# Kernel optimization log

Hardware: AMD Instinct MI355X
Metric: run time of the kernel (lower is better)

Reference implementation:

```python
import jax, jax.numpy as jnp
import numpy as np

B, L, D, H = 4, 2048, 512, 8
HD = D // H
NEG = -1e9


def setup_inputs() -> dict:
    key = jax.random.key(0)
    ks = jax.random.split(key, 11)
    s = 1.0 / np.sqrt(D)
    inp = {
        "q": jax.random.normal(ks[0], (B, L, D), jnp.float32),
        "k": jax.random.normal(ks[1], (B, L, D), jnp.float32),
        "v": jax.random.normal(ks[2], (B, L, D), jnp.float32),
        "mask": jnp.broadcast_to(jnp.tril(jnp.ones((L, L), jnp.int32)), (B, L, L)),
        "Wq": jax.random.normal(ks[3], (D, D), jnp.float32) * s,
        "bq": jax.random.normal(ks[4], (D,), jnp.float32) * s,
        "Wk": jax.random.normal(ks[5], (D, D), jnp.float32) * s,
        "bk": jax.random.normal(ks[6], (D,), jnp.float32) * s,
        "Wv": jax.random.normal(ks[7], (D, D), jnp.float32) * s,
        "bv": jax.random.normal(ks[8], (D,), jnp.float32) * s,
        "Wo": jax.random.normal(ks[9], (D, D), jnp.float32) * s,
        "bo": jax.random.normal(ks[10], (D,), jnp.float32) * s,
    }
    return inp


def reference(q, k, v, mask, Wq, bq, Wk, bk, Wv, bv, Wo, bo):
    # Linear projections (torch Linear: x @ W.T + b)
    Q = (q @ Wq.T + bq).reshape(B, L, H, HD).transpose(0, 2, 1, 3)  # [B,H,L,hd]
    K = (k @ Wk.T + bk).reshape(B, L, H, HD).transpose(0, 2, 1, 3)
    V = (v @ Wv.T + bv).reshape(B, L, H, HD).transpose(0, 2, 1, 3)
    # scaled dot-product attention with masked_fill(mask==0, -1e9)
    score = jnp.einsum('bhqd,bhkd->bhqk', Q, K) / jnp.sqrt(jnp.float32(HD))
    score = jnp.where(mask[:, None, :, :] == 0, NEG, score)
    attn = jax.nn.softmax(score, axis=-1)
    ctx = jnp.einsum('bhqk,bhkd->bhqd', attn, V)  # [B,H,L,hd]
    ctx = ctx.transpose(0, 2, 1, 3).reshape(B, L, D)
    return ctx @ Wo.T + bo
```

## Files before the change

kernel.cpp:

```cpp
#include <hip/hip_runtime.h>
#include <hip/hip_bf16.h>
#include <math.h>

constexpr int Bc  = 4;
constexpr int Lc  = 2048;
constexpr int Dc  = 512;
constexpr int Hc  = 8;
constexpr int HDc = 64;

constexpr int GK = Dc;
constexpr int BK = 64;

typedef __attribute__((ext_vector_type(8))) short bf16x8;
typedef __attribute__((ext_vector_type(4))) short bf16x4;
typedef __attribute__((ext_vector_type(4))) float f32x4;
typedef __attribute__((ext_vector_type(16))) float f32x16;
typedef __attribute__((ext_vector_type(4))) int i32x4;

static __device__ __forceinline__ short f2bf(float x) {
    __hip_bfloat16 h = __float2bfloat16(x);
    return (short)__builtin_bit_cast(unsigned short, h);
}

static __device__ __forceinline__ int cvtpk_bf16(float lo, float hi) {
    int r;
    asm("v_cvt_pk_bf16_f32 %0, %1, %2" : "=v"(r) : "v"(lo), "v"(hi));
    return r;
}

static __device__ __forceinline__ void gload_lds16(const void* g, void* l) {
    __builtin_amdgcn_global_load_lds(
        (const __attribute__((address_space(1))) void*)g,
        (__attribute__((address_space(3))) void*)l, 16, 0, 0);
}

__global__ __launch_bounds__(256)
void cast_all(const float* __restrict__ q, const float* __restrict__ k,
              const float* __restrict__ v, const float* __restrict__ wq,
              const float* __restrict__ wk, const float* __restrict__ wv,
              const float* __restrict__ wo, short* __restrict__ dst) {
    const size_t i = ((size_t)blockIdx.x * 256 + threadIdx.x) * 8;
    const float* src; size_t off;
    if      (i <  4194304) { src = q;  off = i; }
    else if (i <  8388608) { src = k;  off = i -  4194304; }
    else if (i < 12582912) { src = v;  off = i -  8388608; }
    else if (i < 12845056) { src = wq; off = i - 12582912; }
    else if (i < 13107200) { src = wk; off = i - 12845056; }
    else if (i < 13369344) { src = wv; off = i - 13107200; }
    else                   { src = wo; off = i - 13369344; }
    const float4 a = *(const float4*)(src + off);
    const float4 b = *(const float4*)(src + off + 4);
    bf16x8 o;
    o[0] = f2bf(a.x); o[1] = f2bf(a.y); o[2] = f2bf(a.z); o[3] = f2bf(a.w);
    o[4] = f2bf(b.x); o[5] = f2bf(b.y); o[6] = f2bf(b.z); o[7] = f2bf(b.w);
    *(bf16x8*)(dst + i) = o;
}

template<int BM, int BN, int WMT, int WNT>
__device__ __forceinline__ void gemm_tile(const short* __restrict__ A,
                                          const short* __restrict__ W,
                                          short* As, short* Bs,
                                          f32x4 (&acc)[WMT][WNT],
                                          int m0, int n0) {
    const int tid  = threadIdx.x;
    const int w    = tid >> 6;
    const int lane = tid & 63;
    const int low4 = lane & 15;
    const int quad = lane >> 4;
    const int wm   = w & 1, wn = w >> 1;
    const int lrow = lane >> 3;
    const int lchk = (lane & 7) * 8;

    for (int k0 = 0; k0 < GK; k0 += BK) {
#pragma unroll
        for (int i = 0; i < BM / 32; ++i) {
            const int r0 = i * 32 + w * 8;
            gload_lds16(A + (size_t)(m0 + r0 + lrow) * GK + k0 + lchk, As + r0 * BK);
        }
#pragma unroll
        for (int i = 0; i < BN / 32; ++i) {
            const int r0 = i * 32 + w * 8;
            gload_lds16(W + (size_t)(n0 + r0 + lrow) * GK + k0 + lchk, Bs + r0 * BK);
        }
        __syncthreads();
#pragma unroll
        for (int ks = 0; ks < 2; ++ks) {
            bf16x8 af[WMT], bfr[WNT];
#pragma unroll
            for (int mi = 0; mi < WMT; ++mi)
                af[mi] = *(const bf16x8*)(As + (wm * WMT * 16 + mi * 16 + low4) * BK + ks * 32 + quad * 8);
#pragma unroll
            for (int ni = 0; ni < WNT; ++ni)
                bfr[ni] = *(const bf16x8*)(Bs + (wn * WNT * 16 + ni * 16 + low4) * BK + ks * 32 + quad * 8);
#pragma unroll
            for (int mi = 0; mi < WMT; ++mi)
#pragma unroll
                for (int ni = 0; ni < WNT; ++ni)
                    acc[mi][ni] = __builtin_amdgcn_mfma_f32_16x16x32_bf16(af[mi], bfr[ni], acc[mi][ni], 0, 0, 0);
        }
        __syncthreads();
    }
}

__global__ __launch_bounds__(256)
void qkv_gemm(const short* __restrict__ Xq, const short* __restrict__ Xk,
              const short* __restrict__ Xv, const short* __restrict__ Wcat,
              const float* __restrict__ bq, const float* __restrict__ bk,
              const float* __restrict__ bv,
              short* __restrict__ Qw, short* __restrict__ Kw, short* __restrict__ Vw) {
    __shared__ __align__(16) short Smem[128 * 138];
    short* As = Smem;
    short* Bs = Smem + 8192;
    short* Ts = Smem;

    const int tid = threadIdx.x;
    const int i    = blockIdx.x;
    const int slot = i >> 3;
    const int g    = (i & 7) + 8 * (slot >> 2);
    const int j    = slot & 3;
    const int z    = g >> 6;
    const int m0   = (g & 63) * 128;
    const int n0   = z * 512 + j * 128;

    const short* A    = (z == 0) ? Xq : (z == 1) ? Xk : Xv;
    const float* bias = (z == 0) ? bq : (z == 1) ? bk : bv;

    f32x4 acc[4][4];
#pragma unroll
    for (int mi = 0; mi < 4; ++mi)
#pragma unroll
        for (int ni = 0; ni < 4; ++ni) acc[mi][ni] = (f32x4){0.f, 0.f, 0.f, 0.f};

    gemm_tile<128, 128, 4, 4>(A, Wcat, As, Bs, acc, m0, n0);

    const int lane = tid & 63, w = tid >> 6;
    const int low4 = lane & 15, quad = lane >> 4;
    const int wm = w & 1, wn = w >> 1;

    if (z < 2) {
        short* Y = (z == 0) ? Qw : Kw;
        const float qs = (z == 0) ? 0.18033688f : 1.0f;
#pragma unroll
        for (int mi = 0; mi < 4; ++mi)
#pragma unroll
            for (int ni = 0; ni < 4; ++ni)
#pragma unroll
                for (int r = 0; r < 4; ++r) {
                    const int rowL = wm * 64 + mi * 16 + quad * 4 + r;
                    const int colL = wn * 64 + ni * 16 + low4;
                    const int c    = (n0 & 511) + colL;
                    Ts[rowL * 138 + colL] = f2bf((acc[mi][ni][r] + bias[c]) * qs);
                }
        __syncthreads();
        const int jj = tid & 7;
        const int b = m0 >> 11;
#pragma unroll
        for (int it = 0; it < 8; ++it) {
            const int slot2 = it * 32 + (tid >> 3);
            const int row  = slot2 >> 1, half = slot2 & 1;
            const int c0 = (n0 & 511) + half * 64;
            const int h  = c0 >> 6;
            const int l  = (m0 & 2047) + row;
            short* dst = Y + (((size_t)b * Hc + h) * Lc + l) * HDc + jj * 8;
            *(bf16x8*)dst = *(const bf16x8*)(Ts + row * 138 + half * 64 + jj * 8);
        }
    } else {
#pragma unroll
        for (int mi = 0; mi < 4; ++mi)
#pragma unroll
            for (int ni = 0; ni < 4; ++ni)
#pragma unroll
                for (int r = 0; r < 4; ++r) {
                    const int rowL = wm * 64 + mi * 16 + quad * 4 + r;
                    const int colL = wn * 64 + ni * 16 + low4;
                    const int c    = (n0 + colL) & 511;
                    Ts[colL * 136 + rowL] = f2bf(acc[mi][ni][r] + bias[c]);
                }
        __syncthreads();
        const int hdl = tid >> 1, seg = tid & 1;
        const int c  = (n0 + hdl) & 511;
        const int h  = c >> 6, hd = c & 63;
        const int b  = m0 >> 11, l0 = (m0 & 2047) + seg * 64;
        short* dst = Vw + (((size_t)b * Hc + h) * HDc + hd) * Lc + l0;
        const short* srcT = Ts + hdl * 136 + seg * 64;
#pragma unroll
        for (int jj = 0; jj < 8; ++jj)
            *(bf16x8*)(dst + jj * 8) = *(const bf16x8*)(srcT + jj * 8);
    }
}

__global__ __launch_bounds__(256)
void out_gemm(const short* __restrict__ A, const short* __restrict__ W,
              const float* __restrict__ bias, float* __restrict__ Y) {
    __shared__ __align__(16) float SmemF[64 * 132];
    short* As = (short*)SmemF;
    short* Bs = As + 64 * BK;
    float* Tf = SmemF;

    const int tid = threadIdx.x;
    const int i    = blockIdx.x;
    const int slot = i >> 3;
    const int g    = (i & 7) + 8 * (slot >> 2);
    const int j    = slot & 3;
    const int m0   = g * 64;
    const int n0   = j * 128;

    f32x4 acc[2][4];
#pragma unroll
    for (int mi = 0; mi < 2; ++mi)
#pragma unroll
        for (int ni = 0; ni < 4; ++ni) acc[mi][ni] = (f32x4){0.f, 0.f, 0.f, 0.f};

    gemm_tile<64, 128, 2, 4>(A, W, As, Bs, acc, m0, n0);

    const int lane = tid & 63, w = tid >> 6;
    const int low4 = lane & 15, quad = lane >> 4;
    const int wm = w & 1, wn = w >> 1;
#pragma unroll
    for (int mi = 0; mi < 2; ++mi)
#pragma unroll
        for (int ni = 0; ni < 4; ++ni)
#pragma unroll
            for (int r = 0; r < 4; ++r) {
                const int rowL = wm * 32 + mi * 16 + quad * 4 + r;
                const int colL = wn * 64 + ni * 16 + low4;
                Tf[rowL * 132 + colL] = acc[mi][ni][r] + bias[n0 + colL];
            }
    __syncthreads();

    const int c = (tid & 31) * 4;
#pragma unroll
    for (int p = 0; p < 8; ++p) {
        const int row = p * 8 + (tid >> 5);
        *(float4*)(Y + (size_t)(m0 + row) * Dc + n0 + c) =
            *(const float4*)(Tf + row * 132 + c);
    }
}

__global__ __launch_bounds__(256, 4)
void flash_attn(const short* __restrict__ Qb, const short* __restrict__ Kb,
                const short* __restrict__ VTb, short* __restrict__ ctx) {
    __shared__ __align__(16) float CbS[2][2048];
    __shared__ float ClS[2][64];

    const int tid  = threadIdx.x;
    const int w    = tid >> 6;
    const int lane = tid & 63;
    const int t31  = lane & 31;
    const int hh   = lane >> 5;
    const int qcol = w & 1;
    const int kh   = w >> 1;

    const int u  = blockIdx.x;
    const int bh = u & 31;
    const int j  = u >> 5;
    const int a  = (j < 16) ? (31 - j) : (j - 16);
    const int n  = a + 1;
    const int q0 = a * 64 + qcol * 32;

    const short* Qg = Qb  + (size_t)bh * Lc * HDc;
    const short* Kg = Kb  + (size_t)bh * Lc * HDc;
    const short* Vg = VTb + (size_t)bh * HDc * Lc;

    const int bb = bh >> 3, head = bh & 7;
    short* cg = ctx + (size_t)bb * Lc * Dc + (size_t)head * HDc;

    bf16x8 qa[4];
#pragma unroll
    for (int hc = 0; hc < 4; ++hc)
        qa[hc] = *(const bf16x8*)(Qg + (size_t)(q0 + t31) * HDc + hc * 16 + hh * 8);

    f32x16 o0, o1;
#pragma unroll
    for (int i = 0; i < 16; ++i) { o0[i] = 0.f; o1[i] = 0.f; }
    float lps = 0.f;

    const short* krow = Kg + (size_t)(kh * 32 + t31) * HDc + hh * 8;
    const short* vr0  = Vg + (size_t)t31 * Lc        + kh * 32 + hh * 8;
    const short* vr1  = Vg + (size_t)(32 + t31) * Lc + kh * 32 + hh * 8;

    for (int t = 0; t < n; ++t) {
        const bool lastT = (t == a);
        if (lastT && qcol == 0 && kh == 1) break;

        const short* kb = krow + (size_t)t * (64 * HDc);
        bf16x8 kf0 = *(const bf16x8*)(kb);
        bf16x8 kf1 = *(const bf16x8*)(kb + 16);
        bf16x8 kf2 = *(const bf16x8*)(kb + 32);
        bf16x8 kf3 = *(const bf16x8*)(kb + 48);
        f32x16 s;
#pragma unroll
        for (int i = 0; i < 16; ++i) s[i] = 0.f;
        s = __builtin_amdgcn_mfma_f32_32x32x16_bf16(kf0, qa[0], s, 0, 0, 0);
        s = __builtin_amdgcn_mfma_f32_32x32x16_bf16(kf1, qa[1], s, 0, 0, 0);
        s = __builtin_amdgcn_mfma_f32_32x32x16_bf16(kf2, qa[2], s, 0, 0, 0);
        s = __builtin_amdgcn_mfma_f32_32x32x16_bf16(kf3, qa[3], s, 0, 0, 0);

        if (lastT && !(qcol == 1 && kh == 0)) {
            const int qv  = q0 + t31;
            const int kb0 = t * 64 + kh * 32 + 4 * hh;
#pragma unroll
            for (int r = 0; r < 16; ++r) {
                const int kl = kb0 + (r & 3) + 8 * (r >> 2);
                const float p = (kl <= qv) ? exp2f(s[r]) : 0.f;
                lps += p; s[r] = p;
            }
        } else {
#pragma unroll
            for (int r = 0; r < 16; ++r) {
                const float p = exp2f(s[r]);
                lps += p; s[r] = p;
            }
        }

        const short* vb0 = vr0 + t * 64;
        const short* vb1 = vr1 + t * 64;
#pragma unroll
        for (int kc = 0; kc < 2; ++kc) {
            const int g = 8 * kc;
            int u0 = cvtpk_bf16(s[g],     s[g + 1]);
            int u1 = cvtpk_bf16(s[g + 2], s[g + 3]);
            int v0 = cvtpk_bf16(s[g + 4], s[g + 5]);
            int v1 = cvtpk_bf16(s[g + 6], s[g + 7]);
            asm volatile("v_permlane32_swap_b32 %0, %1" : "+v"(u0), "+v"(v0));
            asm volatile("v_permlane32_swap_b32 %0, %1" : "+v"(u1), "+v"(v1));
            i32x4 pw; pw[0] = u0; pw[1] = u1; pw[2] = v0; pw[3] = v1;
            const bf16x8 pa = __builtin_bit_cast(bf16x8, pw);

            const bf16x8 vf0 = *(const bf16x8*)(vb0 + kc * 16);
            const bf16x8 vf1 = *(const bf16x8*)(vb1 + kc * 16);
            o0 = __builtin_amdgcn_mfma_f32_32x32x16_bf16(pa, vf0, o0, 0, 0, 0);
            o1 = __builtin_amdgcn_mfma_f32_32x32x16_bf16(pa, vf1, o1, 0, 0, 0);
        }
    }

    lps += __shfl_xor(lps, 32, 64);

    float* CbX = CbS[qcol];
    float* ClX = ClS[qcol];

    if (kh == 1) {
#pragma unroll
        for (int jj = 0; jj < 4; ++jj) {
            f32x4 a0 = {o0[4 * jj], o0[4 * jj + 1], o0[4 * jj + 2], o0[4 * jj + 3]};
            f32x4 a1 = {o1[4 * jj], o1[4 * jj + 1], o1[4 * jj + 2], o1[4 * jj + 3]};
            *(f32x4*)&CbX[lane * 32 + jj * 4]      = a0;
            *(f32x4*)&CbX[lane * 32 + 16 + jj * 4] = a1;
        }
        ClX[lane] = lps;
    }
    __syncthreads();
    if (kh == 0) {
        lps += ClX[lane];
#pragma unroll
        for (int jj = 0; jj < 4; ++jj) {
            const f32x4 a0 = *(const f32x4*)&CbX[lane * 32 + jj * 4];
            const f32x4 a1 = *(const f32x4*)&CbX[lane * 32 + 16 + jj * 4];
#pragma unroll
            for (int e = 0; e < 4; ++e) {
                o0[4 * jj + e] += a0[e];
                o1[4 * jj + e] += a1[e];
            }
        }
        const float inv = 1.f / lps;
#pragma unroll
        for (int r = 0; r < 16; ++r) {
            const int qloc = (r & 3) + 8 * (r >> 2) + 4 * hh;
            const float iq = __shfl(inv, qloc, 64);
            short* row = cg + (size_t)(q0 + qloc) * Dc;
            row[t31]      = f2bf(o0[r] * iq);
            row[32 + t31] = f2bf(o1[r] * iq);
        }
    }
}

extern "C" void kernel_launch(void* const* d_in, const int* in_sizes, int n_in,
                              void* d_out, int out_size, void* d_ws, size_t ws_size,
                              hipStream_t stream) {
    const float* q  = (const float*)d_in[0];
    const float* k  = (const float*)d_in[1];
    const float* v  = (const float*)d_in[2];
    const float* Wq = (const float*)d_in[4];
    const float* bq = (const float*)d_in[5];
    const float* Wk = (const float*)d_in[6];
    const float* bk = (const float*)d_in[7];
    const float* Wv = (const float*)d_in[8];
    const float* bv = (const float*)d_in[9];
    const float* Wo = (const float*)d_in[10];
    const float* bo = (const float*)d_in[11];
    float* out = (float*)d_out;

    const size_t per = (size_t)Bc * Lc * Dc;
    const size_t wsz = (size_t)Dc * Dc;
    short* Xq   = (short*)d_ws;
    short* Xk   = Xq + per;
    short* Xv   = Xk + per;
    short* Wcat = Xv + per;
    short* Wob  = Wcat + 3 * wsz;
    short* Qw   = Wob + wsz;
    short* Kw   = Qw + per;
    short* Vw   = Kw + per;
    short* Cw   = Vw + per;

    cast_all<<<6656, 256, 0, stream>>>(q, k, v, Wq, Wk, Wv, Wo, Xq);

    qkv_gemm<<<768, 256, 0, stream>>>(Xq, Xk, Xv, Wcat,
                                      bq, bk, bv, Qw, Kw, Vw);

    flash_attn<<<1024, 256, 0, stream>>>(Qw, Kw, Vw, Cw);

    out_gemm<<<512, 256, 0, stream>>>(Cw, Wob, bo, out);
}
```

Baseline: 253.4 us.

## Stage K/V tiles through swizzled per-wave LDS with register prefetch

The attention loop no longer reads K and V fragments straight from global memory in MFMA layout. Each wave now loads its next 32-key K/V tile with coalesced 16-byte loads into registers while computing the current tile. It then commits the tile to a private XOR-swizzled LDS buffer, and MFMA operands are read from there. This is meant to hide global-load latency and cut uncoalesced access, at the cost of 32KB of LDS per block, extra register pressure, and an added barrier before the shared reduction buffer (now aliased onto the same LDS) is reused.

```diff
diff --git a/kernel.cpp b/kernel.cpp
--- a/kernel.cpp
+++ b/kernel.cpp
@@ -240,7 +240,7 @@
 __global__ __launch_bounds__(256, 4)
 void flash_attn(const short* __restrict__ Qb, const short* __restrict__ Kb,
                 const short* __restrict__ VTb, short* __restrict__ ctx) {
-    __shared__ __align__(16) float CbS[2][2048];
+    __shared__ __align__(16) short Smem[16384];
     __shared__ float ClS[2][64];
 
     const int tid  = threadIdx.x;
@@ -248,6 +248,8 @@
     const int lane = tid & 63;
     const int t31  = lane & 31;
     const int hh   = lane >> 5;
+    const int x7   = t31 & 7;
+    const int x3   = t31 & 3;
     const int qcol = w & 1;
     const int kh   = w >> 1;
 
@@ -257,10 +259,21 @@
     const int a  = (j < 16) ? (31 - j) : (j - 16);
     const int n  = a + 1;
     const int q0 = a * 64 + qcol * 32;
+    const int ne = (qcol == 0 && kh == 1) ? (n - 1) : n;
 
     const short* Qg = Qb  + (size_t)bh * Lc * HDc;
-    const short* Kg = Kb  + (size_t)bh * Lc * HDc;
-    const short* Vg = VTb + (size_t)bh * HDc * Lc;
+    const short* Kg = Kb  + (size_t)bh * Lc * HDc + (size_t)(kh * 32) * HDc;
+    const short* Vg = VTb + (size_t)bh * HDc * Lc + kh * 32;
+
+    short* myK = Smem + w * 4096;
+    short* myV = myK + 2048;
+
+    const int grow  = lane >> 3;
+    const int kslot = lane & 7;
+    const int kgch  = kslot ^ grow;
+    const int vrow  = lane >> 2;
+    const int vslot = lane & 3;
+    const int vgch  = vslot ^ (vrow & 3);
 
     const int bb = bh >> 3, head = bh & 7;
     short* cg = ctx + (size_t)bb * Lc * Dc + (size_t)head * HDc;
@@ -275,68 +288,91 @@
     for (int i = 0; i < 16; ++i) { o0[i] = 0.f; o1[i] = 0.f; }
     float lps = 0.f;
 
-    const short* krow = Kg + (size_t)(kh * 32 + t31) * HDc + hh * 8;
-    const short* vr0  = Vg + (size_t)t31 * Lc        + kh * 32 + hh * 8;
-    const short* vr1  = Vg + (size_t)(32 + t31) * Lc + kh * 32 + hh * 8;
-
-    for (int t = 0; t < n; ++t) {
-        const bool lastT = (t == a);
-        if (lastT && qcol == 0 && kh == 1) break;
-
-        const short* kb = krow + (size_t)t * (64 * HDc);
-        bf16x8 kf0 = *(const bf16x8*)(kb);
-        bf16x8 kf1 = *(const bf16x8*)(kb + 16);
-        bf16x8 kf2 = *(const bf16x8*)(kb + 32);
-        bf16x8 kf3 = *(const bf16x8*)(kb + 48);
-        f32x16 s;
-#pragma unroll
-        for (int i = 0; i < 16; ++i) s[i] = 0.f;
-        s = __builtin_amdgcn_mfma_f32_32x32x16_bf16(kf0, qa[0], s, 0, 0, 0);
-        s = __builtin_amdgcn_mfma_f32_32x32x16_bf16(kf1, qa[1], s, 0, 0, 0);
-        s = __builtin_amdgcn_mfma_f32_32x32x16_bf16(kf2, qa[2], s, 0, 0, 0);
-        s = __builtin_amdgcn_mfma_f32_32x32x16_bf16(kf3, qa[3], s, 0, 0, 0);
-
-        if (lastT && !(qcol == 1 && kh == 0)) {
-            const int qv  = q0 + t31;
-            const int kb0 = t * 64 + kh * 32 + 4 * hh;
-#pragma unroll
-            for (int r = 0; r < 16; ++r) {
-                const int kl = kb0 + (r & 3) + 8 * (r >> 2);
-                const float p = (kl <= qv) ? exp2f(s[r]) : 0.f;
-                lps += p; s[r] = p;
+    i32x4 kreg[4], vreg[4];
+
+#define ISSUE(T_)                                                              \
+    {                                                                          \
+        const short* kb_ = Kg + (size_t)(T_) * (64 * HDc);                     \
+        _Pragma("unroll")                                                      \
+        for (int c = 0; c < 4; ++c)                                            \
+            kreg[c] = *(const i32x4*)(kb_ + (c * 8 + grow) * HDc + kgch * 8);  \
+        const short* vb_ = Vg + (T_) * 64;                                     \
+        _Pragma("unroll")                                                      \
+        for (int c = 0; c < 4; ++c)                                            \
+            vreg[c] = *(const i32x4*)(vb_ + (size_t)(c * 16 + vrow) * Lc + vgch * 8); \
+    }
+
+#define COMMIT()                                                               \
+    {                                                                          \
+        _Pragma("unroll")                                                      \
+        for (int c = 0; c < 4; ++c)                                            \
+            *(i32x4*)(myK + (c * 8 + grow) * 64 + kslot * 8) = kreg[c];        \
+        _Pragma("unroll")                                                      \
+        for (int c = 0; c < 4; ++c)                                            \
+            *(i32x4*)(myV + (c * 16 + vrow) * 32 + vslot * 8) = vreg[c];       \
+    }
+
+    if (ne > 0) {
+        ISSUE(0);
+        COMMIT();
+
+        for (int t = 0; t < ne; ++t) {
+            if (t + 1 < ne) ISSUE(t + 1);
+
+            f32x16 s;
+#pragma unroll
+            for (int i = 0; i < 16; ++i) s[i] = 0.f;
+#pragma unroll
+            for (int hc = 0; hc < 4; ++hc) {
+                const int cb = ((hc * 2 + hh) ^ x7) << 3;
+                const bf16x8 kfr = *(const bf16x8*)(myK + t31 * 64 + cb);
+                s = __builtin_amdgcn_mfma_f32_32x32x16_bf16(kfr, qa[hc], s, 0, 0, 0);
             }
-        } else {
-#pragma unroll
-            for (int r = 0; r < 16; ++r) {
-                const float p = exp2f(s[r]);
-                lps += p; s[r] = p;
+
+            if (t == a && !(qcol == 1 && kh == 0)) {
+                const int qv  = q0 + t31;
+                const int kb0 = t * 64 + kh * 32 + 4 * hh;
+#pragma unroll
+                for (int r = 0; r < 16; ++r) {
+                    const int kl = kb0 + (r & 3) + 8 * (r >> 2);
+                    const float p = (kl <= qv) ? exp2f(s[r]) : 0.f;
+                    lps += p; s[r] = p;
+                }
+            } else {
+#pragma unroll
+                for (int r = 0; r < 16; ++r) {
+                    const float p = exp2f(s[r]);
+                    lps += p; s[r] = p;
+                }
             }
-        }
-
-        const short* vb0 = vr0 + t * 64;
-        const short* vb1 = vr1 + t * 64;
-#pragma unroll
-        for (int kc = 0; kc < 2; ++kc) {
-            const int g = 8 * kc;
-            int u0 = cvtpk_bf16(s[g],     s[g + 1]);
-            int u1 = cvtpk_bf16(s[g + 2], s[g + 3]);
-            int v0 = cvtpk_bf16(s[g + 4], s[g + 5]);
-            int v1 = cvtpk_bf16(s[g + 6], s[g + 7]);
-            asm volatile("v_permlane32_swap_b32 %0, %1" : "+v"(u0), "+v"(v0));
-            asm volatile("v_permlane32_swap_b32 %0, %1" : "+v"(u1), "+v"(v1));
-            i32x4 pw; pw[0] = u0; pw[1] = u1; pw[2] = v0; pw[3] = v1;
-            const bf16x8 pa = __builtin_bit_cast(bf16x8, pw);
-
-            const bf16x8 vf0 = *(const bf16x8*)(vb0 + kc * 16);
-            const bf16x8 vf1 = *(const bf16x8*)(vb1 + kc * 16);
-            o0 = __builtin_amdgcn_mfma_f32_32x32x16_bf16(pa, vf0, o0, 0, 0, 0);
-            o1 = __builtin_amdgcn_mfma_f32_32x32x16_bf16(pa, vf1, o1, 0, 0, 0);
+
+#pragma unroll
+            for (int kc = 0; kc < 2; ++kc) {
+                const int g = 8 * kc;
+                int u0 = cvtpk_bf16(s[g],     s[g + 1]);
+                int u1 = cvtpk_bf16(s[g + 2], s[g + 3]);
+                int v0 = cvtpk_bf16(s[g + 4], s[g + 5]);
+                int v1 = cvtpk_bf16(s[g + 6], s[g + 7]);
+                asm volatile("v_permlane32_swap_b32 %0, %1" : "+v"(u0), "+v"(v0));
+                asm volatile("v_permlane32_swap_b32 %0, %1" : "+v"(u1), "+v"(v1));
+                i32x4 pw; pw[0] = u0; pw[1] = u1; pw[2] = v0; pw[3] = v1;
+                const bf16x8 pa = __builtin_bit_cast(bf16x8, pw);
+
+                const int cbv = ((kc * 2 + hh) ^ x3) << 3;
+                const bf16x8 vf0 = *(const bf16x8*)(myV + t31 * 32 + cbv);
+                const bf16x8 vf1 = *(const bf16x8*)(myV + (32 + t31) * 32 + cbv);
+                o0 = __builtin_amdgcn_mfma_f32_32x32x16_bf16(pa, vf0, o0, 0, 0, 0);
+                o1 = __builtin_amdgcn_mfma_f32_32x32x16_bf16(pa, vf1, o1, 0, 0, 0);
+            }
+
+            if (t + 1 < ne) COMMIT();
         }
     }
 
     lps += __shfl_xor(lps, 32, 64);
 
-    float* CbX = CbS[qcol];
+    __syncthreads();
+    float* CbX = (float*)Smem + qcol * 2048;
     float* ClX = ClS[qcol];
 
     if (kh == 1) {
@@ -372,6 +408,8 @@
             row[32 + t31] = f2bf(o1[r] * iq);
         }
     }
+#undef ISSUE
+#undef COMMIT
 }
 
 extern "C" void kernel_launch(void* const* d_in, const int* in_sizes, int n_in,
```

After: 245.1 us. -3.3%, faster.
